# Kernel tuning notes

Hardware: AMD Instinct MI355X
Metric: run time of the kernel (lower is better)

The kernel has to match this reference:

```python
import jax, jax.numpy as jnp
import numpy as np
import math
from jax import lax

HID, H, K = 1024, 8, 4
D = HID // H
B, T = 2, 2048
CLAMP_MAX = 0.999995
LN_EPS = 1e-5

def _logit(x):
    x = min(max(x, 1e-06), 1 - 1e-06)
    return math.log(x / (1 - x))

def setup_inputs() -> dict:
    key = jax.random.key(0)
    ks = jax.random.split(key, 8)
    def xavier(k, fan_in, fan_out):
        s = math.sqrt(2.0 / (fan_in + fan_out))
        return jax.random.normal(k, (fan_in, fan_out), jnp.float32) * s
    x = jax.random.normal(ks[0], (B, T, HID), jnp.float32)
    mask = jnp.ones((B, T), jnp.float32)
    Wq = xavier(ks[1], HID, HID)
    Wk = xavier(ks[2], HID, HID)
    Wv = xavier(ks[3], HID, HID)
    Wb = xavier(ks[4], HID, H)
    bb = jnp.full((H,), _logit(0.99), jnp.float32)
    Wm = xavier(ks[5], HID, H * K)
    bm = jnp.zeros((H * K,), jnp.float32)
    Wo = xavier(ks[6], HID, HID)
    bo = jnp.zeros((HID,), jnp.float32)
    base = np.array([_logit(math.exp(-1.0 / t)) for t in [16.0, 64.0, 256.0, 1024.0]], np.float32)
    base_logit = jnp.asarray(np.tile(base[None, :], (H, 1)))  # (H, K)
    ln_g = jnp.ones((HID,), jnp.float32)
    ln_b = jnp.zeros((HID,), jnp.float32)
    return dict(x=x, mask=mask, Wq=Wq, Wk=Wk, Wv=Wv, Wb=Wb, bb=bb, Wm=Wm, bm=bm,
                Wo=Wo, bo=bo, base_logit=base_logit, ln_g=ln_g, ln_b=ln_b)

def _delta_scan(q, k, v, beta, mix, mask, base_logit):
    # q,k,v: (B,T,H,D); beta: (B,T,H); mix: (B,T,H,K); mask: (B,T)
    b, t = q.shape[0], q.shape[1]
    base_r = jax.nn.sigmoid(base_logit)  # (H,K)
    state0 = jnp.zeros((b, H, K, D, D), jnp.float32)

    def step(state, inp):
        q_t, k_t, v_t, b_t, mix_t, m_t = inp
        valid = (m_t > 0)[:, None, None, None, None]            # (B,1,1,1,1)
        r_eff = jnp.clip(b_t[:, :, None] * base_r[None], 0.0, CLAMP_MAX)  # (B,H,K)
        outer = jnp.einsum('bhd,bhe->bhde', k_t, v_t)[:, :, None]          # (B,H,1,D,D)
        new_state = jnp.where(valid, state * r_eff[..., None, None] + outer, state)
        o_scales = jnp.einsum('bhd,bhkde->bhke', q_t, new_state)           # (B,H,K,D)
        w = jax.nn.softmax(mix_t, axis=-1)                                  # (B,H,K)
        o_t = jnp.sum(w[..., None] * o_scales, axis=2)                      # (B,H,D)
        o_t = o_t * (m_t > 0)[:, None, None].astype(o_t.dtype)
        return new_state, o_t

    xs = (jnp.moveaxis(q, 1, 0), jnp.moveaxis(k, 1, 0), jnp.moveaxis(v, 1, 0),
          jnp.moveaxis(beta, 1, 0), jnp.moveaxis(mix, 1, 0), jnp.moveaxis(mask, 1, 0))
    _, outs = lax.scan(step, state0, xs)       # (T,B,H,D)
    return jnp.moveaxis(outs, 0, 1)            # (B,T,H,D)

def reference(x, mask, Wq, Wk, Wv, Wb, bb, Wm, bm, Wo, bo, base_logit, ln_g, ln_b):
    b, t, _ = x.shape
    def elu1(z):
        return jax.nn.elu(z) + 1.0
    q = elu1((x @ Wq).reshape(b, t, H, D))
    k = elu1((x @ Wk).reshape(b, t, H, D))
    v = (x @ Wv).reshape(b, t, H, D)
    beta = jax.nn.sigmoid(x @ Wb + bb)               # (B,T,H)
    mix = (x @ Wm + bm).reshape(b, t, H, K)          # (B,T,H,K)
    head_out = _delta_scan(q, k, v, beta, mix, mask, base_logit)  # (B,T,H,D)
    out = head_out.reshape(b, t, HID) @ Wo + bo
    y = x + out                                       # residual (dropout in eval mode)
    mu = jnp.mean(y, axis=-1, keepdims=True)
    var = jnp.mean((y - mu) ** 2, axis=-1, keepdims=True)
    return (y - mu) * lax.rsqrt(var + LN_EPS) * ln_g + ln_b
```

## Files before the change

### kernel.cpp

```cpp
#include <hip/hip_runtime.h>
#include <hip/hip_bf16.h>
#include <math.h>

#define TSEQ 2048
#define NHID 1024

typedef float f32x4 __attribute__((ext_vector_type(4)));
typedef __bf16 bf16x8 __attribute__((ext_vector_type(8)));

static __device__ __forceinline__ unsigned short f2bf(float f) {
  unsigned u = __float_as_uint(f);
  u += 0x7fffu + ((u >> 16) & 1u);
  return (unsigned short)(u >> 16);
}
static __device__ __forceinline__ float bf2f(unsigned short h) {
  return __uint_as_float(((unsigned)h) << 16);
}

#define GLDS16(g, l) __builtin_amdgcn_global_load_lds( \
    (const __attribute__((address_space(1))) unsigned int*)(g), \
    (__attribute__((address_space(3))) unsigned int*)(l), 16, 0, 0)

__global__ __launch_bounds__(256) void transpose_all_kernel(
    const float* __restrict__ Wq, const float* __restrict__ Wk,
    const float* __restrict__ Wv, const float* __restrict__ Wo,
    unsigned short* __restrict__ Wqkvt, unsigned short* __restrict__ Wto) {
  __shared__ float tile[32][33];
  const float* W;
  unsigned short* Wt;
  int m = blockIdx.z;
  if (m == 0)      { W = Wq; Wt = Wqkvt; }
  else if (m == 1) { W = Wk; Wt = Wqkvt + 1024 * 1024; }
  else if (m == 2) { W = Wv; Wt = Wqkvt + 2 * 1024 * 1024; }
  else             { W = Wo; Wt = Wto; }
  int bx = blockIdx.x * 32;
  int by = blockIdx.y * 32;
  int tx = threadIdx.x, ty = threadIdx.y;
#pragma unroll
  for (int i = 0; i < 32; i += 8)
    tile[ty + i][tx] = W[(size_t)(by + ty + i) * NHID + bx + tx];
  __syncthreads();
#pragma unroll
  for (int i = 0; i < 32; i += 8)
    Wt[(size_t)(bx + ty + i) * NHID + by + tx] = f2bf(tile[tx][ty + i]);
}

template <int MODE>
__global__ __launch_bounds__(256) void gemm_pipe_kernel(
    const unsigned short* __restrict__ A, const unsigned short* __restrict__ Bt,
    unsigned short* __restrict__ Oq, unsigned short* __restrict__ Ok,
    unsigned short* __restrict__ Ov, float* __restrict__ Pbase) {
  __shared__ __align__(16) unsigned short As[3 * 4096];
  __shared__ __align__(16) unsigned short Bs[3 * 4096];
  const int tid = threadIdx.x;
  const int lane = tid & 63;
  const int wave = tid >> 6;
  const int wr = wave >> 1, wc = wave & 1;
  const int rowBase = blockIdx.y * 128;
  const int colBase = blockIdx.x * 128;
  const int NT = (MODE == 0) ? 32 : 8;
  const int kOff = (MODE == 0) ? 0 : blockIdx.z * 256;

  const int c0 = wave * 128 + lane;
  const int c1 = c0 + 64;
  const int r0 = c0 >> 2, kc0 = (c0 & 3) ^ ((r0 >> 1) & 3);
  const int r1 = c1 >> 2, kc1 = (c1 & 3) ^ ((r1 >> 1) & 3);
  const unsigned short* gA0 = A + (size_t)(rowBase + r0) * 1024 + kOff + kc0 * 8;
  const unsigned short* gA1 = A + (size_t)(rowBase + r1) * 1024 + kOff + kc1 * 8;
  const unsigned short* gB0 = Bt + (size_t)(colBase + r0) * 1024 + kOff + kc0 * 8;
  const unsigned short* gB1 = Bt + (size_t)(colBase + r1) * 1024 + kOff + kc1 * 8;
  const int wofs = wave * 1024;

  const int kq = lane >> 4;
  const int r16 = lane & 15;

  f32x4 acc[4][4] = {};

#define STAGE(buf, k0)                                       \
  do {                                                       \
    GLDS16(gA0 + (k0), &As[(buf) * 4096 + wofs]);            \
    GLDS16(gA1 + (k0), &As[(buf) * 4096 + wofs + 512]);      \
    GLDS16(gB0 + (k0), &Bs[(buf) * 4096 + wofs]);            \
    GLDS16(gB1 + (k0), &Bs[(buf) * 4096 + wofs + 512]);      \
  } while (0)

  STAGE(0, 0);
  STAGE(1, 32);
  int cur = 0, stg = 2;
  for (int t = 0; t < NT; ++t) {
    if (t < NT - 2) {
      STAGE(stg, (t + 2) * 32);
      asm volatile("s_waitcnt vmcnt(8)" ::: "memory");
    } else if (t == NT - 2) {
      asm volatile("s_waitcnt vmcnt(4)" ::: "memory");
    } else {
      asm volatile("s_waitcnt vmcnt(0)" ::: "memory");
    }
    __builtin_amdgcn_s_barrier();
    asm volatile("" ::: "memory");
    const unsigned short* Ac = &As[cur * 4096];
    const unsigned short* Bc = &Bs[cur * 4096];
    bf16x8 af[4], bfr[4];
#pragma unroll
    for (int m = 0; m < 4; ++m) {
      int row = wr * 64 + m * 16 + r16;
      af[m] = *(const bf16x8*)(Ac + row * 32 + (kq ^ ((row >> 1) & 3)) * 8);
      int colr = wc * 64 + m * 16 + r16;
      bfr[m] = *(const bf16x8*)(Bc + colr * 32 + (kq ^ ((colr >> 1) & 3)) * 8);
    }
#pragma unroll
    for (int m = 0; m < 4; ++m)
#pragma unroll
      for (int n = 0; n < 4; ++n)
        acc[m][n] = __builtin_amdgcn_mfma_f32_16x16x32_bf16(af[m], bfr[n], acc[m][n], 0, 0, 0);
    asm volatile("" ::: "memory");
    __builtin_amdgcn_s_barrier();
    asm volatile("" ::: "memory");
    cur = (cur == 2) ? 0 : cur + 1;
    stg = (stg == 2) ? 0 : stg + 1;
  }
#undef STAGE

  const int r4 = (lane >> 4) * 4;
  if (MODE == 1) {
    float* P = Pbase + (size_t)blockIdx.z * 4096 * 1024;
#pragma unroll
    for (int m = 0; m < 4; ++m)
#pragma unroll
      for (int n = 0; n < 4; ++n) {
        int col = colBase + wc * 64 + n * 16 + r16;
#pragma unroll
        for (int j = 0; j < 4; ++j) {
          int row = rowBase + wr * 64 + m * 16 + r4 + j;
          P[(size_t)row * 1024 + col] = acc[m][n][j];
        }
      }
  } else {
    unsigned short* outp;
    int cb;
    bool elu;
    if (colBase < 1024)      { outp = Oq; cb = colBase;        elu = true;  }
    else if (colBase < 2048) { outp = Ok; cb = colBase - 1024; elu = true;  }
    else                     { outp = Ov; cb = colBase - 2048; elu = false; }
#pragma unroll
    for (int m = 0; m < 4; ++m)
#pragma unroll
      for (int n = 0; n < 4; ++n) {
        int col = cb + wc * 64 + n * 16 + r16;
#pragma unroll
        for (int j = 0; j < 4; ++j) {
          int row = rowBase + wr * 64 + m * 16 + r4 + j;
          float v = acc[m][n][j];
          if (elu) v = (v > 0.f) ? (v + 1.f) : expf(v);
          outp[(size_t)row * 1024 + col] = f2bf(v);
        }
      }
  }
}

__global__ __launch_bounds__(256) void pack_wbm_kernel(const float* __restrict__ Wb,
    const float* __restrict__ Wm, float* __restrict__ Wt) {
  int id = blockIdx.x * 256 + threadIdx.x;
  if (id >= 40960) return;
  int o = id >> 10, i = id & 1023;
  Wt[id] = (o < 8) ? Wb[i * 8 + o] : Wm[i * 32 + (o - 8)];
}

__global__ __launch_bounds__(256) void rw8_kernel(const float* __restrict__ x,
    const float* __restrict__ Wt, const float* __restrict__ bb,
    const float* __restrict__ bm, const float* __restrict__ base_logit,
    float* __restrict__ R, float* __restrict__ Wsm,
    unsigned short* __restrict__ Xb) {
  __shared__ float xs[8][1024];
  __shared__ float outs[8][40];
  int row0 = blockIdx.x * 8;
  int tid = threadIdx.x;
#pragma unroll
  for (int r = 0; r < 8; ++r) {
    float4 xv = *(const float4*)(x + (size_t)(row0 + r) * 1024 + tid * 4);
    *(float4*)(&xs[r][tid * 4]) = xv;
    ushort4 xo;
    xo.x = f2bf(xv.x); xo.y = f2bf(xv.y); xo.z = f2bf(xv.z); xo.w = f2bf(xv.w);
    *(ushort4*)(Xb + (size_t)(row0 + r) * 1024 + tid * 4) = xo;
  }
  __syncthreads();
  int wave = tid >> 6, lane = tid & 63;
  for (int o = wave; o < 40; o += 4) {
    const float* wr = Wt + o * 1024;
    float w[16];
#pragma unroll
    for (int it = 0; it < 16; ++it) w[it] = wr[it * 64 + lane];
#pragma unroll
    for (int r = 0; r < 8; ++r) {
      float sum = 0.f;
#pragma unroll
      for (int it = 0; it < 16; ++it) sum += xs[r][it * 64 + lane] * w[it];
#pragma unroll
      for (int off = 32; off > 0; off >>= 1) sum += __shfl_down(sum, off);
      if (lane == 0) outs[r][o] = sum;
    }
  }
  __syncthreads();
  {
    int r = tid >> 5, j = tid & 31;
    int row = row0 + r;
    int h = j >> 2;
    float beta = 1.f / (1.f + expf(-(outs[r][h] + bb[h])));
    float br = 1.f / (1.f + expf(-base_logit[j]));
    float rr = fminf(fmaxf(beta * br, 0.f), 0.999995f);
    float mval = outs[r][8 + j] + bm[j];
    float mx = fmaxf(mval, __shfl_xor(mval, 1));
    mx = fmaxf(mx, __shfl_xor(mx, 2));
    float ex = expf(mval - mx);
    float ssum = ex + __shfl_xor(ex, 1);
    ssum += __shfl_xor(ssum, 2);
    R[(size_t)row * 32 + j] = rr;
    Wsm[(size_t)row * 32 + j] = ex / ssum;
  }
}

__global__ __launch_bounds__(256) void decay2_kernel(const float* __restrict__ R,
    const float* __restrict__ Wsm, const float* __restrict__ mask,
    float* __restrict__ WA, float* __restrict__ IA, float* __restrict__ DU,
    float* __restrict__ AC) {
  int wave = threadIdx.x >> 6, lane = threadIdx.x & 63;
  int id = blockIdx.x * 4 + wave;
  int c = id & 15, k = (id >> 4) & 3, bh = id >> 6;
  int b = bh >> 3, h = bh & 7;
  int row0 = b * TSEQ + c * 128 + 2 * lane;
  float m0 = mask[row0], m1 = mask[row0 + 1];
  size_t i0 = (size_t)row0 * 32 + h * 4 + k;
  float rr0 = (m0 > 0.f) ? R[i0] : 1.f;
  float rr1 = (m1 > 0.f) ? R[i0 + 32] : 1.f;
  float incl = rr0 * rr1;
#pragma unroll
  for (int off = 1; off < 64; off <<= 1) {
    float o = __shfl_up(incl, off);
    if (lane >= off) incl *= o;
  }
  float excl = __shfl_up(incl, 1);
  if (lane == 0) excl = 1.f;
  float a0 = fmaxf(excl * rr0, 1e-25f);
  float a1 = fmaxf(a0 * rr1, 1e-25f);
  float aC = __shfl(a1, 63);
  if (lane == 63) AC[(bh * 16 + c) * 4 + k] = a1;
  bool v0 = m0 > 0.f, v1 = m1 > 0.f;
  float w0 = Wsm[i0], w1 = Wsm[i0 + 32];
  int dub = ((bh * 16 + c) * 4 + k) * 128 + 2 * lane;
  WA[i0] = v0 ? w0 * a0 : 0.f;
  WA[i0 + 32] = v1 ? w1 * a1 : 0.f;
  IA[i0] = v0 ? 1.f / a0 : 0.f;
  IA[i0 + 32] = v1 ? 1.f / a1 : 0.f;
  DU[dub] = v0 ? aC / a0 : 0.f;
  DU[dub + 1] = v1 ? aC / a1 : 0.f;
}

__global__ __launch_bounds__(512) void chunkA_kernel(
    const unsigned short* __restrict__ Qb, const unsigned short* __restrict__ Kb,
    const unsigned short* __restrict__ Vb,
    const float* __restrict__ WA, const float* __restrict__ IA,
    const float* __restrict__ DU,
    unsigned short* __restrict__ Olb, unsigned short* __restrict__ UT) {
  __shared__ __align__(16) char KTl[32768];
  __shared__ __align__(16) char VTl[32768];
  __shared__ __align__(16) char Pl[32768];
  __shared__ __align__(16) float WAl[128][4];
  __shared__ __align__(16) float IAl[128][4];
  __shared__ float DUl[4][128];

  int wg = blockIdx.x;
  int bh = wg >> 4, c = wg & 15;
  int b = bh >> 3, h = bh & 7;
  int t0 = c * 128;
  int tid = threadIdx.x;
  int lane = tid & 63, wave = tid >> 6;
  int wbase = wave * 16;
  int l15 = lane & 15, lq = lane >> 4;

  const size_t qkvbase = ((size_t)b * TSEQ + t0) * 1024 + h * 128;

  for (int it = 0; it < 4; ++it) {
    int ci = tid + it * 512;
    int t = ci >> 4, s = ci & 15;
    bf16x8 kv = *(const bf16x8*)(Kb + qkvbase + (size_t)t * 1024 + s * 8);
    bf16x8 vv = *(const bf16x8*)(Vb + qkvbase + (size_t)t * 1024 + s * 8);
#pragma unroll
    for (int e = 0; e < 8; ++e) {
      int d = s * 8 + e;
      int off = d * 256 + (((t >> 3) ^ (d & 7)) << 4) + (t & 7) * 2;
      *(unsigned short*)(KTl + off) = f2bf((float)kv[e]);
      *(unsigned short*)(VTl + off) = f2bf((float)vv[e]);
    }
  }
  {
    int t = tid >> 2, k = tid & 3;
    size_t idx = ((size_t)b * TSEQ + t0 + t) * 32 + h * 4 + k;
    WAl[t][k] = WA[idx];
    IAl[t][k] = IA[idx];
    int k2 = tid >> 7, j = tid & 127;
    DUl[k2][j] = DU[((bh * 16 + c) * 4 + k2) * 128 + j];
  }
  __syncthreads();

  bf16x8 qf[4];
#pragma unroll
  for (int ds = 0; ds < 4; ++ds)
    qf[ds] = *(const bf16x8*)(Qb + qkvbase + (size_t)(wbase + l15) * 1024 + ds * 32 + lq * 8);
  f32x4 accP[8];
#pragma unroll
  for (int jf = 0; jf < 8; ++jf) {
    f32x4 a = {};
#pragma unroll
    for (int ds = 0; ds < 4; ++ds) {
      bf16x8 kfrag = *(const bf16x8*)(Kb + qkvbase + (size_t)(jf * 16 + l15) * 1024 + ds * 32 + lq * 8);
      a = __builtin_amdgcn_mfma_f32_16x16x32_bf16(qf[ds], kfrag, a, 0, 0, 0);
    }
    accP[jf] = a;
  }

  float4 wa4[4];
#pragma unroll
  for (int jj = 0; jj < 4; ++jj)
    wa4[jj] = *(const float4*)&WAl[wbase + lq * 4 + jj][0];
#pragma unroll
  for (int jf = 0; jf < 8; ++jf) {
    float4 ia4 = *(const float4*)&IAl[jf * 16 + l15][0];
#pragma unroll
    for (int jj = 0; jj < 4; ++jj) {
      int tl = wbase + lq * 4 + jj;
      int jl = jf * 16 + l15;
      float m = 0.f;
      if (jl <= tl)
        m = wa4[jj].x * ia4.x + wa4[jj].y * ia4.y + wa4[jj].z * ia4.z + wa4[jj].w * ia4.w;
      float pv = accP[jf][jj] * m;
      int off = tl * 256 + (((jl >> 3) ^ (tl & 7)) << 4) + (jl & 7) * 2;
      *(unsigned short*)(Pl + off) = f2bf(pv);
    }
  }

  bf16x8 pf[4];
#pragma unroll
  for (int js = 0; js < 4; ++js) {
    int tl = wbase + l15;
    int slot = js * 4 + lq;
    pf[js] = *(const bf16x8*)(Pl + tl * 256 + ((slot ^ (tl & 7)) << 4));
  }
#pragma unroll
  for (int dvf = 0; dvf < 8; ++dvf) {
    f32x4 a = {};
    int dv = dvf * 16 + l15;
#pragma unroll
    for (int js = 0; js < 4; ++js) {
      int slot = js * 4 + lq;
      bf16x8 vfrag = *(const bf16x8*)(VTl + dv * 256 + ((slot ^ (dv & 7)) << 4));
      a = __builtin_amdgcn_mfma_f32_16x16x32_bf16(pf[js], vfrag, a, 0, 0, 0);
    }
#pragma unroll
    for (int jj = 0; jj < 4; ++jj) {
      int tl = wbase + lq * 4 + jj;
      Olb[((size_t)b * TSEQ + t0 + tl) * 1024 + h * 128 + dv] = f2bf(a[jj]);
    }
  }

  if (c < 15) {
#pragma unroll 1
    for (int k = 0; k < 4; ++k) {
      f32x4 accU[8] = {};
#pragma unroll 1
      for (int js = 0; js < 4; ++js) {
        int dvr = wbase + l15;
        int slot = js * 4 + lq;
        bf16x8 af = *(const bf16x8*)(VTl + dvr * 256 + ((slot ^ (dvr & 7)) << 4));
        int j0 = js * 32 + lq * 8;
        bf16x8 afs;
#pragma unroll
        for (int e = 0; e < 8; ++e)
          afs[e] = (__bf16)((float)af[e] * DUl[k][j0 + e]);
#pragma unroll
        for (int dkf = 0; dkf < 8; ++dkf) {
          int dk = dkf * 16 + l15;
          bf16x8 kf = *(const bf16x8*)(KTl + dk * 256 + ((slot ^ (dk & 7)) << 4));
          accU[dkf] = __builtin_amdgcn_mfma_f32_16x16x32_bf16(afs, kf, accU[dkf], 0, 0, 0);
        }
      }
      size_t ub = (((size_t)bh * 16 + c) * 4 + k) * 16384;
#pragma unroll
      for (int dkf = 0; dkf < 8; ++dkf) {
        int dk = dkf * 16 + l15;
#pragma unroll
        for (int jj = 0; jj < 4; ++jj) {
          int dvr = wbase + lq * 4 + jj;
          UT[ub + (size_t)dvr * 128 + dk] = f2bf(accU[dkf][jj]);
        }
      }
    }
  }
}

__global__ __launch_bounds__(256) void chainB_kernel(const unsigned short* __restrict__ UT,
    const float* __restrict__ AC, unsigned short* __restrict__ S0T) {
  int id = blockIdx.x * 256 + threadIdx.x;
  int dk = id & 127;
  int dv = (id >> 7) & 127;
  int k = (id >> 14) & 3;
  int bh = id >> 16;
  size_t elem = (size_t)dv * 128 + dk;
  float S = 0.f;
#pragma unroll 1
  for (int c = 0; c < 15; ++c) {
    size_t ub = (((size_t)bh * 16 + c) * 4 + k) * 16384;
    float u = bf2f(UT[ub + elem]);
    float aC = AC[(bh * 16 + c) * 4 + k];
    S = aC * S + u;
    size_t sb = (((size_t)bh * 16 + (c + 1)) * 4 + k) * 16384;
    S0T[sb + elem] = f2bf(S);
  }
}

__global__ __launch_bounds__(512) void chunkC_kernel(const unsigned short* __restrict__ Qb,
    const unsigned short* __restrict__ S0T, const float* __restrict__ WA,
    const unsigned short* __restrict__ Olb, unsigned short* __restrict__ Ob) {
  __shared__ __align__(16) char Sl[32768];
  int wg = blockIdx.x;
  int bh = wg >> 4, c = wg & 15;
  int b = bh >> 3, h = bh & 7;
  int t0 = c * 128;
  int tid = threadIdx.x, lane = tid & 63, wave = tid >> 6;
  int l15 = lane & 15, lq = lane >> 4, wbase = wave * 16;
  size_t qbase = ((size_t)b * TSEQ + t0) * 1024 + h * 128;

  f32x4 accO[8] = {};
  if (c > 0) {
    int tl = wbase + l15;
#pragma unroll 1
    for (int k = 0; k < 4; ++k) {
      __syncthreads();
      size_t sb = (((size_t)bh * 16 + c) * 4 + k) * 16384;
      for (int it = 0; it < 4; ++it) {
        int ci = tid + it * 512;
        int dv = ci >> 4, s = ci & 15;
        bf16x8 vv = *(const bf16x8*)(S0T + sb + (size_t)dv * 128 + s * 8);
        *(bf16x8*)(Sl + dv * 256 + ((s ^ (dv & 7)) << 4)) = vv;
      }
      __syncthreads();
      float sc = WA[((size_t)b * TSEQ + t0 + tl) * 32 + h * 4 + k];
#pragma unroll 1
      for (int ds = 0; ds < 4; ++ds) {
        bf16x8 qf = *(const bf16x8*)(Qb + qbase + (size_t)tl * 1024 + ds * 32 + lq * 8);
        bf16x8 qs;
#pragma unroll
        for (int e = 0; e < 8; ++e) qs[e] = (__bf16)((float)qf[e] * sc);
#pragma unroll
        for (int dvf = 0; dvf < 8; ++dvf) {
          int dv = dvf * 16 + l15;
          int slot = ds * 4 + lq;
          bf16x8 sf = *(const bf16x8*)(Sl + dv * 256 + ((slot ^ (dv & 7)) << 4));
          accO[dvf] = __builtin_amdgcn_mfma_f32_16x16x32_bf16(qs, sf, accO[dvf], 0, 0, 0);
        }
      }
    }
  }
#pragma unroll
  for (int dvf = 0; dvf < 8; ++dvf) {
    int dv = dvf * 16 + l15;
#pragma unroll
    for (int jj = 0; jj < 4; ++jj) {
      int tl = wbase + lq * 4 + jj;
      size_t off = ((size_t)b * TSEQ + t0 + tl) * 1024 + h * 128 + dv;
      Ob[off] = f2bf(accO[dvf][jj] + bf2f(Olb[off]));
    }
  }
}

__global__ __launch_bounds__(256) void ln_kernel(const float* __restrict__ Pbase,
    const float* __restrict__ bo, const float* __restrict__ xres,
    const float* __restrict__ g, const float* __restrict__ bta,
    float* __restrict__ out) {
  int row = blockIdx.x;
  int tid = threadIdx.x;
  int lane = tid & 63, wave = tid >> 6;
  __shared__ float red[8];
  size_t base = (size_t)row * 1024 + tid * 4;
  const size_t PS = (size_t)4096 * 1024;
  float4 a = *(const float4*)(Pbase + base);
  float4 b2 = *(const float4*)(Pbase + PS + base);
  float4 c2 = *(const float4*)(Pbase + 2 * PS + base);
  float4 d2 = *(const float4*)(Pbase + 3 * PS + base);
  float4 xv = *(const float4*)(xres + base);
  float4 bv = *(const float4*)(bo + tid * 4);
  float4 v;
  v.x = ((a.x + b2.x) + (c2.x + d2.x)) + bv.x + xv.x;
  v.y = ((a.y + b2.y) + (c2.y + d2.y)) + bv.y + xv.y;
  v.z = ((a.z + b2.z) + (c2.z + d2.z)) + bv.z + xv.z;
  v.w = ((a.w + b2.w) + (c2.w + d2.w)) + bv.w + xv.w;
  float sum = v.x + v.y + v.z + v.w;
#pragma unroll
  for (int off = 32; off > 0; off >>= 1) sum += __shfl_down(sum, off);
  if (lane == 0) red[wave] = sum;
  __syncthreads();
  float mu = (red[0] + red[1] + red[2] + red[3]) * (1.f / 1024.f);
  float4 d;
  d.x = v.x - mu; d.y = v.y - mu; d.z = v.z - mu; d.w = v.w - mu;
  float sq = d.x * d.x + d.y * d.y + d.z * d.z + d.w * d.w;
#pragma unroll
  for (int off = 32; off > 0; off >>= 1) sq += __shfl_down(sq, off);
  __syncthreads();
  if (lane == 0) red[4 + wave] = sq;
  __syncthreads();
  float var = (red[4] + red[5] + red[6] + red[7]) * (1.f / 1024.f);
  float inv = rsqrtf(var + 1e-5f);
  float4 gg = *(const float4*)(g + tid * 4);
  float4 bb4 = *(const float4*)(bta + tid * 4);
  float4 o;
  o.x = d.x * inv * gg.x + bb4.x;
  o.y = d.y * inv * gg.y + bb4.y;
  o.z = d.z * inv * gg.z + bb4.z;
  o.w = d.w * inv * gg.w + bb4.w;
  *(float4*)(out + (size_t)row * 1024 + tid * 4) = o;
}

extern "C" void kernel_launch(void* const* d_in, const int* in_sizes, int n_in,
                              void* d_out, int out_size, void* d_ws, size_t ws_size,
                              hipStream_t stream) {
  const float* x    = (const float*)d_in[0];
  const float* mask = (const float*)d_in[1];
  const float* Wq   = (const float*)d_in[2];
  const float* Wk   = (const float*)d_in[3];
  const float* Wv   = (const float*)d_in[4];
  const float* Wb   = (const float*)d_in[5];
  const float* bb   = (const float*)d_in[6];
  const float* Wm   = (const float*)d_in[7];
  const float* bm   = (const float*)d_in[8];
  const float* Wo   = (const float*)d_in[9];
  const float* bo   = (const float*)d_in[10];
  const float* base_logit = (const float*)d_in[11];
  const float* ln_g = (const float*)d_in[12];
  const float* ln_b = (const float*)d_in[13];

  char* ws = (char*)d_ws;
  const size_t MB = 1024u * 1024u;
  unsigned short* Xb    = (unsigned short*)(ws + 0);
  unsigned short* Wqkvt = (unsigned short*)(ws + 8 * MB);
  unsigned short* Wto   = (unsigned short*)(ws + 14 * MB);
  float* Rf  = (float*)(ws + 16 * MB);
  float* Wsf = (float*)(ws + 16 * MB + 512 * 1024);
  float* WAf = (float*)(ws + 17 * MB);
  float* IAf = (float*)(ws + 17 * MB + 512 * 1024);
  float* DUf = (float*)(ws + 18 * MB);
  float* ACf = (float*)(ws + 18 * MB + 512 * 1024);
  float* Wtf = (float*)(ws + 18 * MB + 768 * 1024);
  unsigned short* Qb  = (unsigned short*)(ws + 19 * MB);
  unsigned short* Kb  = (unsigned short*)(ws + 27 * MB);
  unsigned short* Vb  = (unsigned short*)(ws + 35 * MB);
  unsigned short* Olb = (unsigned short*)(ws + 43 * MB);
  unsigned short* Ob  = (unsigned short*)(ws + 51 * MB);
  unsigned short* UTb = (unsigned short*)(ws + 59 * MB);
  unsigned short* S0T = (unsigned short*)(ws + 91 * MB);
  float* Pp = (float*)(ws + 59 * MB);
  if (ws_size < 131 * MB) return;

  dim3 tb(32, 8), tg(32, 32, 4);
  transpose_all_kernel<<<tg, tb, 0, stream>>>(Wq, Wk, Wv, Wo, Wqkvt, Wto);
  pack_wbm_kernel<<<160, 256, 0, stream>>>(Wb, Wm, Wtf);

  rw8_kernel<<<512, 256, 0, stream>>>(x, Wtf, bb, bm, base_logit, Rf, Wsf, Xb);
  decay2_kernel<<<256, 256, 0, stream>>>(Rf, Wsf, mask, WAf, IAf, DUf, ACf);

  dim3 gqkv(24, 32);
  gemm_pipe_kernel<0><<<gqkv, 256, 0, stream>>>(Xb, Wqkvt, Qb, Kb, Vb, nullptr);

  chunkA_kernel<<<256, 512, 0, stream>>>(Qb, Kb, Vb, WAf, IAf, DUf, Olb, UTb);
  chainB_kernel<<<4096, 256, 0, stream>>>(UTb, ACf, S0T);
  chunkC_kernel<<<256, 512, 0, stream>>>(Qb, S0T, WAf, Olb, Ob);

  dim3 gwo(8, 32, 4);
  gemm_pipe_kernel<1><<<gwo, 256, 0, stream>>>(Ob, Wto, nullptr, nullptr, nullptr, Pp);

  ln_kernel<<<4096, 256, 0, stream>>>(Pp, bo, x, ln_g, ln_b, (float*)d_out);
}
```

Measured before the change: 182.7 us.

## Merge weight-pack launch, halve Wo split-K, and pack K/V LDS transposes

The Wb/Wm packing kernel is folded into the transpose kernel as an extra z-slice, which removes one launch. The output-projection GEMM now splits K in two slices of 512 instead of four of 256, so the layernorm kernel reads two partial buffers instead of four. The chunkA K/V transpose into LDS now loads two timesteps and writes packed 32-bit pairs with an extra XOR swizzle term, cutting LDS store count and bank conflicts. The tradeoff is fewer workgroups for the Wo GEMM (512 instead of 1024), which may reduce occupancy.

```diff
diff --git a/kernel.cpp b/kernel.cpp
--- a/kernel.cpp
+++ b/kernel.cpp
@@ -24,18 +24,28 @@
 __global__ __launch_bounds__(256) void transpose_all_kernel(
     const float* __restrict__ Wq, const float* __restrict__ Wk,
     const float* __restrict__ Wv, const float* __restrict__ Wo,
-    unsigned short* __restrict__ Wqkvt, unsigned short* __restrict__ Wto) {
+    const float* __restrict__ Wb, const float* __restrict__ Wm,
+    unsigned short* __restrict__ Wqkvt, unsigned short* __restrict__ Wto,
+    float* __restrict__ Wtf) {
+  int m = blockIdx.z;
+  int tx = threadIdx.x, ty = threadIdx.y;
+  if (m == 4) {
+    int blk = blockIdx.y * 32 + blockIdx.x;
+    if (blk >= 160) return;
+    int id = blk * 256 + ty * 32 + tx;
+    int o = id >> 10, i = id & 1023;
+    Wtf[id] = (o < 8) ? Wb[i * 8 + o] : Wm[i * 32 + (o - 8)];
+    return;
+  }
   __shared__ float tile[32][33];
   const float* W;
   unsigned short* Wt;
-  int m = blockIdx.z;
   if (m == 0)      { W = Wq; Wt = Wqkvt; }
   else if (m == 1) { W = Wk; Wt = Wqkvt + 1024 * 1024; }
   else if (m == 2) { W = Wv; Wt = Wqkvt + 2 * 1024 * 1024; }
   else             { W = Wo; Wt = Wto; }
   int bx = blockIdx.x * 32;
   int by = blockIdx.y * 32;
-  int tx = threadIdx.x, ty = threadIdx.y;
 #pragma unroll
   for (int i = 0; i < 32; i += 8)
     tile[ty + i][tx] = W[(size_t)(by + ty + i) * NHID + bx + tx];
@@ -58,8 +68,8 @@
   const int wr = wave >> 1, wc = wave & 1;
   const int rowBase = blockIdx.y * 128;
   const int colBase = blockIdx.x * 128;
-  const int NT = (MODE == 0) ? 32 : 8;
-  const int kOff = (MODE == 0) ? 0 : blockIdx.z * 256;
+  const int NT = (MODE == 0) ? 32 : 16;
+  const int kOff = (MODE == 0) ? 0 : blockIdx.z * 512;
 
   const int c0 = wave * 128 + lane;
   const int c1 = c0 + 64;
@@ -156,14 +166,6 @@
         }
       }
   }
-}
-
-__global__ __launch_bounds__(256) void pack_wbm_kernel(const float* __restrict__ Wb,
-    const float* __restrict__ Wm, float* __restrict__ Wt) {
-  int id = blockIdx.x * 256 + threadIdx.x;
-  if (id >= 40960) return;
-  int o = id >> 10, i = id & 1023;
-  Wt[id] = (o < 8) ? Wb[i * 8 + o] : Wm[i * 32 + (o - 8)];
 }
 
 __global__ __launch_bounds__(256) void rw8_kernel(const float* __restrict__ x,
@@ -255,6 +257,8 @@
   DU[dub + 1] = v1 ? aC / a1 : 0.f;
 }
 
+#define KV_SLOT(j, d) (((j) ^ ((d) & 7) ^ (((d) >> 3) & 7)) << 4)
+
 __global__ __launch_bounds__(512) void chunkA_kernel(
     const unsigned short* __restrict__ Qb, const unsigned short* __restrict__ Kb,
     const unsigned short* __restrict__ Vb,
@@ -279,17 +283,23 @@
 
   const size_t qkvbase = ((size_t)b * TSEQ + t0) * 1024 + h * 128;
 
-  for (int it = 0; it < 4; ++it) {
+  for (int it = 0; it < 2; ++it) {
     int ci = tid + it * 512;
-    int t = ci >> 4, s = ci & 15;
-    bf16x8 kv = *(const bf16x8*)(Kb + qkvbase + (size_t)t * 1024 + s * 8);
-    bf16x8 vv = *(const bf16x8*)(Vb + qkvbase + (size_t)t * 1024 + s * 8);
+    int t = (ci >> 4) * 2, s = ci & 15;
+    bf16x8 k0 = *(const bf16x8*)(Kb + qkvbase + (size_t)t * 1024 + s * 8);
+    bf16x8 k1 = *(const bf16x8*)(Kb + qkvbase + (size_t)(t + 1) * 1024 + s * 8);
+    bf16x8 v0 = *(const bf16x8*)(Vb + qkvbase + (size_t)t * 1024 + s * 8);
+    bf16x8 v1 = *(const bf16x8*)(Vb + qkvbase + (size_t)(t + 1) * 1024 + s * 8);
+    const unsigned short* k0u = (const unsigned short*)&k0;
+    const unsigned short* k1u = (const unsigned short*)&k1;
+    const unsigned short* v0u = (const unsigned short*)&v0;
+    const unsigned short* v1u = (const unsigned short*)&v1;
 #pragma unroll
     for (int e = 0; e < 8; ++e) {
       int d = s * 8 + e;
-      int off = d * 256 + (((t >> 3) ^ (d & 7)) << 4) + (t & 7) * 2;
-      *(unsigned short*)(KTl + off) = f2bf((float)kv[e]);
-      *(unsigned short*)(VTl + off) = f2bf((float)vv[e]);
+      int off = d * 256 + (((t >> 3) ^ (d & 7) ^ ((d >> 3) & 7)) << 4) + (t & 7) * 2;
+      *(unsigned int*)(KTl + off) = (unsigned)k0u[e] | ((unsigned)k1u[e] << 16);
+      *(unsigned int*)(VTl + off) = (unsigned)v0u[e] | ((unsigned)v1u[e] << 16);
     }
   }
   {
@@ -352,7 +362,7 @@
 #pragma unroll
     for (int js = 0; js < 4; ++js) {
       int slot = js * 4 + lq;
-      bf16x8 vfrag = *(const bf16x8*)(VTl + dv * 256 + ((slot ^ (dv & 7)) << 4));
+      bf16x8 vfrag = *(const bf16x8*)(VTl + dv * 256 + KV_SLOT(slot, dv));
       a = __builtin_amdgcn_mfma_f32_16x16x32_bf16(pf[js], vfrag, a, 0, 0, 0);
     }
 #pragma unroll
@@ -370,7 +380,7 @@
       for (int js = 0; js < 4; ++js) {
         int dvr = wbase + l15;
         int slot = js * 4 + lq;
-        bf16x8 af = *(const bf16x8*)(VTl + dvr * 256 + ((slot ^ (dvr & 7)) << 4));
+        bf16x8 af = *(const bf16x8*)(VTl + dvr * 256 + KV_SLOT(slot, dvr));
         int j0 = js * 32 + lq * 8;
         bf16x8 afs;
 #pragma unroll
@@ -379,7 +389,7 @@
 #pragma unroll
         for (int dkf = 0; dkf < 8; ++dkf) {
           int dk = dkf * 16 + l15;
-          bf16x8 kf = *(const bf16x8*)(KTl + dk * 256 + ((slot ^ (dk & 7)) << 4));
+          bf16x8 kf = *(const bf16x8*)(KTl + dk * 256 + KV_SLOT(slot, dk));
           accU[dkf] = __builtin_amdgcn_mfma_f32_16x16x32_bf16(afs, kf, accU[dkf], 0, 0, 0);
         }
       }
@@ -484,15 +494,13 @@
   const size_t PS = (size_t)4096 * 1024;
   float4 a = *(const float4*)(Pbase + base);
   float4 b2 = *(const float4*)(Pbase + PS + base);
-  float4 c2 = *(const float4*)(Pbase + 2 * PS + base);
-  float4 d2 = *(const float4*)(Pbase + 3 * PS + base);
   float4 xv = *(const float4*)(xres + base);
   float4 bv = *(const float4*)(bo + tid * 4);
   float4 v;
-  v.x = ((a.x + b2.x) + (c2.x + d2.x)) + bv.x + xv.x;
-  v.y = ((a.y + b2.y) + (c2.y + d2.y)) + bv.y + xv.y;
-  v.z = ((a.z + b2.z) + (c2.z + d2.z)) + bv.z + xv.z;
-  v.w = ((a.w + b2.w) + (c2.w + d2.w)) + bv.w + xv.w;
+  v.x = a.x + b2.x + bv.x + xv.x;
+  v.y = a.y + b2.y + bv.y + xv.y;
+  v.z = a.z + b2.z + bv.z + xv.z;
+  v.w = a.w + b2.w + bv.w + xv.w;
   float sum = v.x + v.y + v.z + v.w;
 #pragma unroll
   for (int off = 32; off > 0; off >>= 1) sum += __shfl_down(sum, off);
@@ -559,9 +567,8 @@
   float* Pp = (float*)(ws + 59 * MB);
   if (ws_size < 131 * MB) return;
 
-  dim3 tb(32, 8), tg(32, 32, 4);
-  transpose_all_kernel<<<tg, tb, 0, stream>>>(Wq, Wk, Wv, Wo, Wqkvt, Wto);
-  pack_wbm_kernel<<<160, 256, 0, stream>>>(Wb, Wm, Wtf);
+  dim3 tb(32, 8), tg(32, 32, 5);
+  transpose_all_kernel<<<tg, tb, 0, stream>>>(Wq, Wk, Wv, Wo, Wb, Wm, Wqkvt, Wto, Wtf);
 
   rw8_kernel<<<512, 256, 0, stream>>>(x, Wtf, bb, bm, base_logit, Rf, Wsf, Xb);
   decay2_kernel<<<256, 256, 0, stream>>>(Rf, Wsf, mask, WAf, IAf, DUf, ACf);
@@ -573,7 +580,7 @@
   chainB_kernel<<<4096, 256, 0, stream>>>(UTb, ACf, S0T);
   chunkC_kernel<<<256, 512, 0, stream>>>(Qb, S0T, WAf, Olb, Ob);
 
-  dim3 gwo(8, 32, 4);
+  dim3 gwo(8, 32, 2);
   gemm_pipe_kernel<1><<<gwo, 256, 0, stream>>>(Ob, Wto, nullptr, nullptr, nullptr, Pp);
 
   ln_kernel<<<4096, 256, 0, stream>>>(Pp, bo, x, ln_g, ln_b, (float*)d_out);
```

New measurement: 168.9 us. 1.08x faster.
